# Optimization experiments

Measured on AMD Instinct MI355X. Metric: run time of the kernel, lower is better.

Reference implementation:

```python
import jax, jax.numpy as jnp
from jax import lax
import numpy as np

B, S, D, H2, V = 1024, 256, 128, 5, 50257
EPS = 1e-5


def setup_inputs() -> dict:
    key = jax.random.key(0)
    ks = jax.random.split(key, 12)
    s = 0.08  # init scale ~ 1/sqrt(D)
    return {
        "x": jax.random.randint(ks[0], (B, S), 0, V),
        "emb": jax.random.normal(ks[1], (V, D), jnp.float32) * s,
        "W_ih1": jax.random.normal(ks[2], (D, D), jnp.float32) * s,
        "b_ih1": jax.random.normal(ks[3], (D,), jnp.float32) * s,
        "W_hh1": jax.random.normal(ks[4], (D, D), jnp.float32) * s,
        "b_hh1": jax.random.normal(ks[5], (D,), jnp.float32) * s,
        "g1": jnp.ones((D,), jnp.float32),
        "be1": jnp.zeros((D,), jnp.float32),
        "W_ih2": jax.random.normal(ks[6], (H2, D), jnp.float32) * s,
        "b_ih2": jax.random.normal(ks[7], (H2,), jnp.float32) * s,
        "W_hh2": jax.random.normal(ks[8], (H2, H2), jnp.float32) * s,
        "b_hh2": jax.random.normal(ks[9], (H2,), jnp.float32) * s,
        "g2": jnp.ones((H2,), jnp.float32),
        "be2": jnp.zeros((H2,), jnp.float32),
    }


def _rnn(xproj, W_hh):
    """Vanilla tanh RNN. xproj: [B,S,H] = x @ W_ih^T + b_ih + b_hh (precomputed)."""
    h0 = jnp.zeros((xproj.shape[0], W_hh.shape[0]), xproj.dtype)

    def step(h, xt):  # xt: [B,H]
        h = jnp.tanh(xt + h @ W_hh.T)
        return h, h

    _, hs = lax.scan(step, h0, jnp.swapaxes(xproj, 0, 1))  # [S,B,H]
    return jnp.swapaxes(hs, 0, 1)  # [B,S,H]


def _ln(z, g, b):
    m = jnp.mean(z, axis=-1, keepdims=True)
    v = jnp.mean(jnp.square(z - m), axis=-1, keepdims=True)
    return (z - m) * lax.rsqrt(v + EPS) * g + b


def reference(x, emb, W_ih1, b_ih1, W_hh1, b_hh1, g1, be1,
              W_ih2, b_ih2, W_hh2, b_hh2, g2, be2):
    e = emb[x]  # [B,S,D]
    z = _rnn(e @ W_ih1.T + (b_ih1 + b_hh1), W_hh1)
    z = _ln(z, g1, be1)
    z = _rnn(z @ W_ih2.T + (b_ih2 + b_hh2), W_hh2)  # [B,S,5]
    z = _ln(z, g2, be2)
    pooled = jnp.mean(z, axis=1)  # AvgPool1d over full seq -> [B,5]
    return jax.nn.softmax(pooled, axis=1)
```

## Files before the change

### kernel.cpp

```cpp
#include <hip/hip_runtime.h>
#include <stdint.h>

#define S_LEN 256
#define DIM   128
#define EPSL  1e-5f

typedef __bf16 bf16x8 __attribute__((ext_vector_type(8)));
typedef float  f32x4  __attribute__((ext_vector_type(4)));

__device__ __forceinline__ unsigned short f2bf_bits(float f) {
  union { float f; unsigned int u; } v; v.f = f;
  unsigned int r = v.u + 0x7fffu + ((v.u >> 16) & 1u);
  return (unsigned short)(r >> 16);
}
__device__ __forceinline__ float bf2f_bits(unsigned short b) {
  union { float f; unsigned int u; } v; v.u = ((unsigned int)b) << 16; return v.f;
}
__device__ __forceinline__ unsigned f2bf_rhu(float f) {
  return (__float_as_uint(f) + 0x8000u) >> 16;
}
__device__ __forceinline__ unsigned pack_rhu(float lo, float hi) {
  return __builtin_amdgcn_perm(__float_as_uint(hi) + 0x8000u,
                               __float_as_uint(lo) + 0x8000u, 0x07060302u);
}
__device__ __forceinline__ float tanh_fast(float x) {
  float e = __expf(2.f * x);
  return 1.f - 2.f * __builtin_amdgcn_rcpf(e + 1.f);
}

template<int CTRL>
__device__ __forceinline__ float dpp_rot_add(float v) {
  int r = __builtin_amdgcn_update_dpp(0, __float_as_int(v), CTRL, 0xF, 0xF, true);
  return v + __int_as_float(r);
}
template<int CTRL>
__device__ __forceinline__ float dpp_rot_max(float v) {
  int r = __builtin_amdgcn_update_dpp(0, __float_as_int(v), CTRL, 0xF, 0xF, true);
  return fmaxf(v, __int_as_float(r));
}
__device__ __forceinline__ float dpp_sum16(float v) {
  v = dpp_rot_add<0x124>(v); v = dpp_rot_add<0x128>(v);
  v = dpp_rot_add<0x39>(v);  v = dpp_rot_add<0x4E>(v);
  return v;
}
__device__ __forceinline__ float dpp_max16(float v) {
  v = dpp_rot_max<0x124>(v); v = dpp_rot_max<0x128>(v);
  v = dpp_rot_max<0x39>(v);  v = dpp_rot_max<0x4E>(v);
  return v;
}
template<int CTRL>
__device__ __forceinline__ void red_level7(float& s, float& sq, float* d) {
  s  = dpp_rot_add<CTRL>(s);
  sq = dpp_rot_add<CTRL>(sq);
#pragma unroll
  for (int j = 0; j < 5; j++) d[j] = dpp_rot_add<CTRL>(d[j]);
}
template<int JJ>
__device__ __forceinline__ float bcast16(float v) {
  int r = __builtin_amdgcn_ds_swizzle(__float_as_int(v), (JJ << 5) | 0x10);
  return __int_as_float(r);
}

union Frag8 { unsigned short us[8]; bf16x8 v; int4 i4; };

__global__ __launch_bounds__(512, 2)
void rnn_main(const int* __restrict__ x, const float* __restrict__ emb,
              const float* __restrict__ Wih1, const float* __restrict__ bih1,
              const float* __restrict__ Whh1, const float* __restrict__ bhh1,
              const float* __restrict__ g1, const float* __restrict__ be1,
              const float* __restrict__ Wih2, const float* __restrict__ bih2,
              const float* __restrict__ Whh2, const float* __restrict__ bhh2,
              const float* __restrict__ g2, const float* __restrict__ be2,
              unsigned short* __restrict__ hout, int* flags,
              float* __restrict__ out)
{
  __shared__ __align__(16) unsigned short h_bf[2][16 * 128];
  __shared__ __align__(16) unsigned short e_bf[2][16 * 128];
  __shared__ int x_tile[16 * 256];
  __shared__ __align__(16) float p_lds[8][2][32][8];

  const int tid  = threadIdx.x;
  const int wave = tid >> 6;
  const int lane = tid & 63;
  const int l15  = lane & 15;
  const int q    = lane >> 4;

  if (blockIdx.x < 64) {
    const int r0 = blockIdx.x * 16;
    for (int i = tid; i < 16 * 256; i += 512)
      x_tile[i] = x[(size_t)(r0 + (i >> 8)) * S_LEN + (i & 255)];
    for (int i = tid; i < 16 * 128; i += 512) h_bf[1][i] = 0;

    const int n1 = wave * 16 + l15;
    const float bias1v = bih1[n1] + bhh1[n1];
    bf16x8 wh[4], wih[4];
#pragma unroll
    for (int kt = 0; kt < 4; kt++) {
      int k0 = kt * 32 + q * 8;
      Frag8 fh, fa;
#pragma unroll
      for (int j = 0; j < 8; j++) {
        fh.us[j] = f2bf_bits(Whh1[n1 * DIM + k0 + j]);
        fa.us[j] = f2bf_bits(Wih1[n1 * DIM + k0 + j]);
      }
      wh[kt] = fh.v; wih[kt] = fa.v;
    }

    const bool stage_role = (wave >= 4);
    float pf[2][8];
    const int gm   = (wave & 3) * 4 + q;
    const int goct = l15;
    const int gdst = gm * 128 + ((goct ^ gm) & 15) * 8;
    __syncthreads();

    if (stage_role) {
      float ta[8], tb[8];
      { int xid = x_tile[gm * 256 + 0];
        const float* pe = emb + (size_t)xid * DIM + goct * 8;
#pragma unroll
        for (int j = 0; j < 8; j++) ta[j] = pe[j]; }
      { int xid = x_tile[gm * 256 + 1];
        const float* pe = emb + (size_t)xid * DIM + goct * 8;
#pragma unroll
        for (int j = 0; j < 8; j++) tb[j] = pe[j]; }
      { int xid = x_tile[gm * 256 + 2];
        const float* pe = emb + (size_t)xid * DIM + goct * 8;
#pragma unroll
        for (int j = 0; j < 8; j++) pf[0][j] = pe[j]; }
      { int xid = x_tile[gm * 256 + 3];
        const float* pe = emb + (size_t)xid * DIM + goct * 8;
#pragma unroll
        for (int j = 0; j < 8; j++) pf[1][j] = pe[j]; }
      Frag8 pa, pb;
#pragma unroll
      for (int j = 0; j < 8; j++) { pa.us[j] = f2bf_bits(ta[j]); pb.us[j] = f2bf_bits(tb[j]); }
      *(int4*)&e_bf[0][gdst] = pa.i4;
      *(int4*)&e_bf[1][gdst] = pb.i4;
    }
    __syncthreads();

    f32x4 xpacc = {bias1v, bias1v, bias1v, bias1v};
#pragma unroll
    for (int kt = 0; kt < 4; kt++) {
      int sw = (((kt * 4 + q) ^ l15) & 15) * 8;
      bf16x8 ae = *(const bf16x8*)&e_bf[0][l15 * 128 + sw];
      xpacc = __builtin_amdgcn_mfma_f32_16x16x32_bf16(ae, wih[kt], xpacc, 0, 0, 0);
    }
    asm volatile("s_waitcnt lgkmcnt(0)\n\ts_barrier" ::: "memory");

#pragma unroll 2
    for (int t = 0; t < S_LEN; t++) {
      f32x4 acc = xpacc;
      {
        const int rb = (t + 1) & 1;
#pragma unroll
        for (int kt = 0; kt < 4; kt++) {
          int sw = (((kt * 4 + q) ^ l15) & 15) * 8;
          bf16x8 ahf = *(const bf16x8*)&h_bf[rb][l15 * 128 + sw];
          acc = __builtin_amdgcn_mfma_f32_16x16x32_bf16(ahf, wh[kt], acc, 0, 0, 0);
        }
        const int wb = t & 1;
        const int oct = n1 >> 3;
#pragma unroll
        for (int r = 0; r < 4; r++) {
          int row = q * 4 + r;
          unsigned short us = (unsigned short)f2bf_rhu(tanh_fast(acc[r]));
          h_bf[wb][row * 128 + ((oct ^ row) & 15) * 8 + (n1 & 7)] = us;
          hout[((size_t)(r0 + row) * S_LEN + t) * DIM + n1] = us;
        }
      }

      if (t + 1 < S_LEN) {
        f32x4 a = {bias1v, bias1v, bias1v, bias1v};
#pragma unroll
        for (int kt = 0; kt < 4; kt++) {
          int sw = (((kt * 4 + q) ^ l15) & 15) * 8;
          bf16x8 ae = *(const bf16x8*)&e_bf[(t + 1) & 1][l15 * 128 + sw];
          a = __builtin_amdgcn_mfma_f32_16x16x32_bf16(ae, wih[kt], a, 0, 0, 0);
        }
        xpacc = a;
      }

      if (stage_role) {
        if (t + 2 < S_LEN) {
          int4 pk;
          pk.x = pack_rhu(pf[t & 1][0], pf[t & 1][1]);
          pk.y = pack_rhu(pf[t & 1][2], pf[t & 1][3]);
          pk.z = pack_rhu(pf[t & 1][4], pf[t & 1][5]);
          pk.w = pack_rhu(pf[t & 1][6], pf[t & 1][7]);
          *(int4*)&e_bf[t & 1][gdst] = pk;
        }
        if (t + 4 < S_LEN) {
          int xid = x_tile[gm * 256 + t + 4];
          const float* pe = emb + (size_t)xid * DIM + goct * 8;
#pragma unroll
          for (int j = 0; j < 8; j++) pf[t & 1][j] = pe[j];
        }
      }
      if (flags != nullptr && (t & 31) == 31)
        asm volatile("s_waitcnt vmcnt(0)" ::: "memory");
      asm volatile("s_waitcnt lgkmcnt(0)\n\ts_barrier" ::: "memory");
      if (flags != nullptr && (t & 31) == 31 && tid == 0)
        __hip_atomic_store(&flags[blockIdx.x * 8 + (t >> 5)], (t >> 5) + 1,
                           __ATOMIC_RELEASE, __HIP_MEMORY_SCOPE_AGENT);
    }
  } else {
    const int bt = blockIdx.x - 64;
    float w2g[5][8], Gs[5], Bs[5], wrow[5];
#pragma unroll
    for (int j = 0; j < 8; j++) {
      int c = l15 * 8 + j;
      float gc = g1[c];
#pragma unroll
      for (int jj = 0; jj < 5; jj++) w2g[jj][j] = Wih2[jj * DIM + c] * gc;
    }
#pragma unroll
    for (int jj = 0; jj < 5; jj++) { Gs[jj] = 0.f; Bs[jj] = 0.f; }
    for (int c = 0; c < DIM; c++) {
      float gc = g1[c], bc = be1[c];
#pragma unroll
      for (int jj = 0; jj < 5; jj++) {
        float w = Wih2[jj * DIM + c];
        Gs[jj] += w * gc; Bs[jj] += w * bc;
      }
    }
    const float validf = (l15 < 5) ? 1.f : 0.f;
    float t2_l = 0.f, g2_l = 0.f, be2_l = 0.f;
    if (l15 < 5) {
      t2_l = bih2[l15] + bhh2[l15];
      g2_l = g2[l15]; be2_l = be2[l15];
#pragma unroll
      for (int jj = 0; jj < 5; jj++) wrow[jj] = Whh2[l15 * 5 + jj];
    } else {
#pragma unroll
      for (int jj = 0; jj < 5; jj++) wrow[jj] = 0.f;
    }
    float h2rep[5] = {0, 0, 0, 0, 0}, pool_l = 0.f;
    const int row_l = 2 * wave + (q & 1);
    const unsigned short* hb =
        hout + (size_t)(bt * 16 + row_l) * S_LEN * DIM;
    const int idx = (l15 < 5) ? l15 : 0;

    for (int c8 = 0; c8 < 8; c8++) {
      if (tid == 0) {
        while (__hip_atomic_load(&flags[bt * 8 + c8], __ATOMIC_RELAXED,
                                 __HIP_MEMORY_SCOPE_AGENT) < c8 + 1)
          __builtin_amdgcn_s_sleep(2);
      }
      __syncthreads();
      __builtin_amdgcn_fence(__ATOMIC_ACQUIRE, "agent");
      for (int tt = 0; tt < 16; tt++) {
        int toff = tt * 2 + (q >> 1);
        uint4 cur = *(const uint4*)(hb + (size_t)(c8 * 32 + toff) * DIM + l15 * 8);
        float hv[8];
        hv[0] = __uint_as_float(cur.x << 16); hv[1] = __uint_as_float(cur.x & 0xffff0000u);
        hv[2] = __uint_as_float(cur.y << 16); hv[3] = __uint_as_float(cur.y & 0xffff0000u);
        hv[4] = __uint_as_float(cur.z << 16); hv[5] = __uint_as_float(cur.z & 0xffff0000u);
        hv[6] = __uint_as_float(cur.w << 16); hv[7] = __uint_as_float(cur.w & 0xffff0000u);
        float s = 0.f, sq = 0.f, d[5] = {0, 0, 0, 0, 0};
#pragma unroll
        for (int j = 0; j < 8; j++) {
          float v = hv[j];
          s += v; sq += v * v;
#pragma unroll
          for (int jj = 0; jj < 5; jj++) d[jj] = fmaf(w2g[jj][j], v, d[jj]);
        }
        red_level7<0x124>(s, sq, d);
        red_level7<0x128>(s, sq, d);
        red_level7<0x39>(s, sq, d);
        red_level7<0x4E>(s, sq, d);
        float mean = s * (1.f / 128.f);
        float var  = sq * (1.f / 128.f) - mean * mean;
        float rstd = rsqrtf(var + EPSL);
        float p[5];
#pragma unroll
        for (int jj = 0; jj < 5; jj++)
          p[jj] = rstd * (d[jj] - mean * Gs[jj]) + Bs[jj];
        float psel = (l15 == 0) ? p[0] : (l15 == 1) ? p[1] :
                     (l15 == 2) ? p[2] : (l15 == 3) ? p[3] : p[4];
        if (l15 < 5) p_lds[wave][q & 1][toff][l15] = psel;
      }
      asm volatile("s_waitcnt lgkmcnt(0)" ::: "memory");
      for (int s = 0; s < 32; s++) {
        float pv = p_lds[wave][q & 1][s][idx];
        float a = pv + t2_l;
#pragma unroll
        for (int jj = 0; jj < 5; jj++) a = fmaf(wrow[jj], h2rep[jj], a);
        float xn = tanh_fast(a);
        float s2 = dpp_sum16(xn * validf) * 0.2f;
        float dd = xn - s2;
        float v2 = dpp_sum16(dd * dd * validf) * 0.2f;
        float r2 = rsqrtf(v2 + EPSL);
        pool_l += dd * r2 * g2_l + be2_l;
        h2rep[0] = bcast16<0>(xn); h2rep[1] = bcast16<1>(xn);
        h2rep[2] = bcast16<2>(xn); h2rep[3] = bcast16<3>(xn);
        h2rep[4] = bcast16<4>(xn);
      }
    }
    float lg = pool_l * (1.f / 256.f);
    float mx = dpp_max16((l15 < 5) ? lg : -3.0e38f);
    float e  = (l15 < 5) ? __expf(lg - mx) : 0.f;
    float sm = dpp_sum16(e);
    if (q < 2 && l15 < 5)
      out[(size_t)(bt * 16 + row_l) * 5 + l15] = e / sm;
  }
}

__global__ __launch_bounds__(256, 2)
void rnn_tail_r11(const unsigned short* __restrict__ hall,
                  const float* __restrict__ g1,  const float* __restrict__ be1,
                  const float* __restrict__ Wih2, const float* __restrict__ bih2,
                  const float* __restrict__ Whh2, const float* __restrict__ bhh2,
                  const float* __restrict__ g2,  const float* __restrict__ be2,
                  float* __restrict__ out)
{
  __shared__ float p_lds[4][4][8];
  const int tid  = threadIdx.x;
  const int wave = tid >> 6;
  const int lane = tid & 63;
  const int l15  = lane & 15;
  const int q    = lane >> 4;
  const int b    = blockIdx.x * 4 + wave;

  float w2g[5][8], Gs[5], Bs[5], wrow[5];
#pragma unroll
  for (int j = 0; j < 8; j++) {
    int c = l15 * 8 + j;
    float gc = g1[c];
#pragma unroll
    for (int jj = 0; jj < 5; jj++) w2g[jj][j] = Wih2[jj * DIM + c] * gc;
  }
#pragma unroll
  for (int jj = 0; jj < 5; jj++) { Gs[jj] = 0.f; Bs[jj] = 0.f; }
  for (int c = 0; c < DIM; c++) {
    float gc = g1[c], bc = be1[c];
#pragma unroll
    for (int jj = 0; jj < 5; jj++) {
      float w = Wih2[jj * DIM + c];
      Gs[jj] += w * gc; Bs[jj] += w * bc;
    }
  }
  const float validf = (l15 < 5) ? 1.f : 0.f;
  float t2_l = 0.f, g2_l = 0.f, be2_l = 0.f;
  if (l15 < 5) {
    t2_l = bih2[l15] + bhh2[l15];
    g2_l = g2[l15]; be2_l = be2[l15];
#pragma unroll
    for (int jj = 0; jj < 5; jj++) wrow[jj] = Whh2[l15 * 5 + jj];
  } else {
#pragma unroll
    for (int jj = 0; jj < 5; jj++) wrow[jj] = 0.f;
  }
  float h2rep[5];
#pragma unroll
  for (int jj = 0; jj < 5; jj++) h2rep[jj] = 0.f;
  float pool_l = 0.f;

  const unsigned short* hb = hall + (size_t)b * S_LEN * DIM;
  uint4 hpre = *(const uint4*)(hb + (size_t)q * DIM + l15 * 8);

  for (int t0 = 0; t0 < S_LEN; t0 += 4) {
    uint4 cur = hpre;
    if (t0 + 4 < S_LEN)
      hpre = *(const uint4*)(hb + (size_t)(t0 + 4 + q) * DIM + l15 * 8);
    float hv[8];
    hv[0] = __uint_as_float(cur.x << 16); hv[1] = __uint_as_float(cur.x & 0xffff0000u);
    hv[2] = __uint_as_float(cur.y << 16); hv[3] = __uint_as_float(cur.y & 0xffff0000u);
    hv[4] = __uint_as_float(cur.z << 16); hv[5] = __uint_as_float(cur.z & 0xffff0000u);
    hv[6] = __uint_as_float(cur.w << 16); hv[7] = __uint_as_float(cur.w & 0xffff0000u);
    float s = 0.f, sq = 0.f, d[5] = {0, 0, 0, 0, 0};
#pragma unroll
    for (int j = 0; j < 8; j++) {
      float v = hv[j];
      s += v; sq += v * v;
#pragma unroll
      for (int jj = 0; jj < 5; jj++) d[jj] = fmaf(w2g[jj][j], v, d[jj]);
    }
    red_level7<0x124>(s, sq, d);
    red_level7<0x128>(s, sq, d);
    red_level7<0x39>(s, sq, d);
    red_level7<0x4E>(s, sq, d);
    float mean = s * (1.f / 128.f);
    float var  = sq * (1.f / 128.f) - mean * mean;
    float rstd = rsqrtf(var + EPSL);
    float p[5];
#pragma unroll
    for (int jj = 0; jj < 5; jj++)
      p[jj] = rstd * (d[jj] - mean * Gs[jj]) + Bs[jj];
    float psel = (l15 == 0) ? p[0] : (l15 == 1) ? p[1] :
                 (l15 == 2) ? p[2] : (l15 == 3) ? p[3] : p[4];
    if (l15 < 5) p_lds[wave][q][l15] = psel;
    asm volatile("s_waitcnt lgkmcnt(0)" ::: "memory");
    const int idx = (l15 < 5) ? l15 : 0;
#pragma unroll
    for (int g = 0; g < 4; g++) {
      float pv = p_lds[wave][g][idx];
      float a = pv + t2_l;
#pragma unroll
      for (int jj = 0; jj < 5; jj++) a = fmaf(wrow[jj], h2rep[jj], a);
      float xn = tanh_fast(a);
      float s2 = dpp_sum16(xn * validf) * 0.2f;
      float dd = xn - s2;
      float v2 = dpp_sum16(dd * dd * validf) * 0.2f;
      float r2 = rsqrtf(v2 + EPSL);
      pool_l += dd * r2 * g2_l + be2_l;
      h2rep[0] = bcast16<0>(xn); h2rep[1] = bcast16<1>(xn);
      h2rep[2] = bcast16<2>(xn); h2rep[3] = bcast16<3>(xn);
      h2rep[4] = bcast16<4>(xn);
    }
  }

  float lg = pool_l * (1.f / 256.f);
  float mx = dpp_max16((l15 < 5) ? lg : -3.0e38f);
  float e  = (l15 < 5) ? __expf(lg - mx) : 0.f;
  float sm = dpp_sum16(e);
  if (q == 0 && l15 < 5) out[(size_t)b * 5 + l15] = e / sm;
}

extern "C" void kernel_launch(void* const* d_in, const int* in_sizes, int n_in,
                              void* d_out, int out_size, void* d_ws, size_t ws_size,
                              hipStream_t stream) {
  (void)in_sizes; (void)n_in; (void)out_size;
  const int*   x    = (const int*)  d_in[0];
  const float* emb  = (const float*)d_in[1];
  const float* Wih1 = (const float*)d_in[2];
  const float* bih1 = (const float*)d_in[3];
  const float* Whh1 = (const float*)d_in[4];
  const float* bhh1 = (const float*)d_in[5];
  const float* g1   = (const float*)d_in[6];
  const float* be1  = (const float*)d_in[7];
  const float* Wih2 = (const float*)d_in[8];
  const float* bih2 = (const float*)d_in[9];
  const float* Whh2 = (const float*)d_in[10];
  const float* bhh2 = (const float*)d_in[11];
  const float* g2   = (const float*)d_in[12];
  const float* be2  = (const float*)d_in[13];
  float* out = (float*)d_out;

  const size_t HBYTES = (size_t)1024 * S_LEN * DIM * 2;
  const size_t FBYTES = 64 * 8 * sizeof(int);
  unsigned short* hws = (unsigned short*)d_ws;

  if (ws_size >= HBYTES + 4096) {
    int* flags = (int*)((char*)d_ws + HBYTES);
    rnn_main<<<dim3(128), dim3(512), 0, stream>>>(
        x, emb, Wih1, bih1, Whh1, bhh1, g1, be1,
        Wih2, bih2, Whh2, bhh2, g2, be2, hws, flags, out);
    (void)FBYTES;
  } else {
    rnn_main<<<dim3(64), dim3(512), 0, stream>>>(
        x, emb, Wih1, bih1, Whh1, bhh1, g1, be1,
        Wih2, bih2, Whh2, bhh2, g2, be2, hws, nullptr, out);
    rnn_tail_r11<<<dim3(256), dim3(256), 0, stream>>>(
        hws, g1, be1, Wih2, bih2, Whh2, bhh2, g2, be2, out);
  }
}
```

Measured before the change: 257.1 us.

## Split recurrence and input projection into separate wave groups with 1024-thread blocks

Doubles the block to 16 waves. Waves 0-7 now only run the recurrent h@W_hh MFMA chain. Waves 8-15 compute the next step's input projection and stage embeddings, handing it over through a new double-buffered xp_lds buffer. The recurrent chain also splits its four MFMAs into two independent accumulators to shorten the dependency chain. In exchange, the per-step barrier now spans 16 waves and each step adds an LDS round-trip. Half the waves in the consumer blocks sit idle.

```diff
diff --git a/kernel.cpp b/kernel.cpp
--- a/kernel.cpp
+++ b/kernel.cpp
@@ -63,57 +63,67 @@
 
 union Frag8 { unsigned short us[8]; bf16x8 v; int4 i4; };
 
-__global__ __launch_bounds__(512, 2)
-void rnn_main(const int* __restrict__ x, const float* __restrict__ emb,
-              const float* __restrict__ Wih1, const float* __restrict__ bih1,
-              const float* __restrict__ Whh1, const float* __restrict__ bhh1,
-              const float* __restrict__ g1, const float* __restrict__ be1,
-              const float* __restrict__ Wih2, const float* __restrict__ bih2,
-              const float* __restrict__ Whh2, const float* __restrict__ bhh2,
-              const float* __restrict__ g2, const float* __restrict__ be2,
-              unsigned short* __restrict__ hout, int* flags,
-              float* __restrict__ out)
+__global__ __launch_bounds__(1024, 4)
+void rnn_main2(const int* __restrict__ x, const float* __restrict__ emb,
+               const float* __restrict__ Wih1, const float* __restrict__ bih1,
+               const float* __restrict__ Whh1, const float* __restrict__ bhh1,
+               const float* __restrict__ g1, const float* __restrict__ be1,
+               const float* __restrict__ Wih2, const float* __restrict__ bih2,
+               const float* __restrict__ Whh2, const float* __restrict__ bhh2,
+               const float* __restrict__ g2, const float* __restrict__ be2,
+               unsigned short* __restrict__ hout, int* flags,
+               float* __restrict__ out)
 {
   __shared__ __align__(16) unsigned short h_bf[2][16 * 128];
   __shared__ __align__(16) unsigned short e_bf[2][16 * 128];
   __shared__ int x_tile[16 * 256];
+  __shared__ __align__(16) float xp_lds[2][128][16];
   __shared__ __align__(16) float p_lds[8][2][32][8];
 
-  const int tid  = threadIdx.x;
-  const int wave = tid >> 6;
-  const int lane = tid & 63;
-  const int l15  = lane & 15;
-  const int q    = lane >> 4;
+  const int tid   = threadIdx.x;
+  const int wave  = tid >> 6;
+  const int waveu = __builtin_amdgcn_readfirstlane(wave);
+  const int lane  = tid & 63;
+  const int l15   = lane & 15;
+  const int q     = lane >> 4;
 
   if (blockIdx.x < 64) {
     const int r0 = blockIdx.x * 16;
-    for (int i = tid; i < 16 * 256; i += 512)
+    for (int i = tid; i < 16 * 256; i += 1024)
       x_tile[i] = x[(size_t)(r0 + (i >> 8)) * S_LEN + (i & 255)];
-    for (int i = tid; i < 16 * 128; i += 512) h_bf[1][i] = 0;
-
-    const int n1 = wave * 16 + l15;
-    const float bias1v = bih1[n1] + bhh1[n1];
-    bf16x8 wh[4], wih[4];
-#pragma unroll
-    for (int kt = 0; kt < 4; kt++) {
-      int k0 = kt * 32 + q * 8;
-      Frag8 fh, fa;
-#pragma unroll
-      for (int j = 0; j < 8; j++) {
-        fh.us[j] = f2bf_bits(Whh1[n1 * DIM + k0 + j]);
-        fa.us[j] = f2bf_bits(Wih1[n1 * DIM + k0 + j]);
-      }
-      wh[kt] = fh.v; wih[kt] = fa.v;
-    }
-
-    const bool stage_role = (wave >= 4);
-    float pf[2][8];
+    for (int i = tid; i < 16 * 128; i += 1024) h_bf[1][i] = 0;
+
+    const int n1 = (waveu < 8 ? wave : wave - 8) * 16 + l15;
+    bf16x8 wreg[4];
+    float bias1v = 0.f;
+    if (waveu < 8) {
+#pragma unroll
+      for (int kt = 0; kt < 4; kt++) {
+        int k0 = kt * 32 + q * 8;
+        Frag8 f;
+#pragma unroll
+        for (int j = 0; j < 8; j++) f.us[j] = f2bf_bits(Whh1[n1 * DIM + k0 + j]);
+        wreg[kt] = f.v;
+      }
+    } else {
+      bias1v = bih1[n1] + bhh1[n1];
+#pragma unroll
+      for (int kt = 0; kt < 4; kt++) {
+        int k0 = kt * 32 + q * 8;
+        Frag8 f;
+#pragma unroll
+        for (int j = 0; j < 8; j++) f.us[j] = f2bf_bits(Wih1[n1 * DIM + k0 + j]);
+        wreg[kt] = f.v;
+      }
+    }
+
     const int gm   = (wave & 3) * 4 + q;
     const int goct = l15;
     const int gdst = gm * 128 + ((goct ^ gm) & 15) * 8;
+    float pf[2][8];
     __syncthreads();
 
-    if (stage_role) {
+    if (waveu >= 8 && waveu < 12) {
       float ta[8], tb[8];
       { int xid = x_tile[gm * 256 + 0];
         const float* pe = emb + (size_t)xid * DIM + goct * 8;
@@ -139,25 +149,38 @@
     }
     __syncthreads();
 
-    f32x4 xpacc = {bias1v, bias1v, bias1v, bias1v};
-#pragma unroll
-    for (int kt = 0; kt < 4; kt++) {
-      int sw = (((kt * 4 + q) ^ l15) & 15) * 8;
-      bf16x8 ae = *(const bf16x8*)&e_bf[0][l15 * 128 + sw];
-      xpacc = __builtin_amdgcn_mfma_f32_16x16x32_bf16(ae, wih[kt], xpacc, 0, 0, 0);
-    }
-    asm volatile("s_waitcnt lgkmcnt(0)\n\ts_barrier" ::: "memory");
+    if (waveu >= 8) {
+      f32x4 a = {bias1v, bias1v, bias1v, bias1v};
+#pragma unroll
+      for (int kt = 0; kt < 4; kt++) {
+        int sw = (((kt * 4 + q) ^ l15) & 15) * 8;
+        bf16x8 ae = *(const bf16x8*)&e_bf[0][l15 * 128 + sw];
+        a = __builtin_amdgcn_mfma_f32_16x16x32_bf16(ae, wreg[kt], a, 0, 0, 0);
+      }
+      *(f32x4*)&xp_lds[0][n1][q * 4] = a;
+    }
+    __syncthreads();
 
 #pragma unroll 2
     for (int t = 0; t < S_LEN; t++) {
-      f32x4 acc = xpacc;
-      {
+      if (waveu < 8) {
         const int rb = (t + 1) & 1;
-#pragma unroll
-        for (int kt = 0; kt < 4; kt++) {
-          int sw = (((kt * 4 + q) ^ l15) & 15) * 8;
-          bf16x8 ahf = *(const bf16x8*)&h_bf[rb][l15 * 128 + sw];
-          acc = __builtin_amdgcn_mfma_f32_16x16x32_bf16(ahf, wh[kt], acc, 0, 0, 0);
+        f32x4 acc  = *(const f32x4*)&xp_lds[t & 1][n1][q * 4];
+        f32x4 accb = {0.f, 0.f, 0.f, 0.f};
+        {
+          int sw0 = ((q ^ l15) & 15) * 8;
+          int sw1 = (((4 + q) ^ l15) & 15) * 8;
+          int sw2 = (((8 + q) ^ l15) & 15) * 8;
+          int sw3 = (((12 + q) ^ l15) & 15) * 8;
+          bf16x8 a0 = *(const bf16x8*)&h_bf[rb][l15 * 128 + sw0];
+          bf16x8 a1 = *(const bf16x8*)&h_bf[rb][l15 * 128 + sw1];
+          bf16x8 a2 = *(const bf16x8*)&h_bf[rb][l15 * 128 + sw2];
+          bf16x8 a3 = *(const bf16x8*)&h_bf[rb][l15 * 128 + sw3];
+          acc  = __builtin_amdgcn_mfma_f32_16x16x32_bf16(a0, wreg[0], acc,  0, 0, 0);
+          accb = __builtin_amdgcn_mfma_f32_16x16x32_bf16(a2, wreg[2], accb, 0, 0, 0);
+          acc  = __builtin_amdgcn_mfma_f32_16x16x32_bf16(a1, wreg[1], acc,  0, 0, 0);
+          accb = __builtin_amdgcn_mfma_f32_16x16x32_bf16(a3, wreg[3], accb, 0, 0, 0);
+          acc += accb;
         }
         const int wb = t & 1;
         const int oct = n1 >> 3;
@@ -168,36 +191,35 @@
           h_bf[wb][row * 128 + ((oct ^ row) & 15) * 8 + (n1 & 7)] = us;
           hout[((size_t)(r0 + row) * S_LEN + t) * DIM + n1] = us;
         }
-      }
-
-      if (t + 1 < S_LEN) {
-        f32x4 a = {bias1v, bias1v, bias1v, bias1v};
-#pragma unroll
-        for (int kt = 0; kt < 4; kt++) {
-          int sw = (((kt * 4 + q) ^ l15) & 15) * 8;
-          bf16x8 ae = *(const bf16x8*)&e_bf[(t + 1) & 1][l15 * 128 + sw];
-          a = __builtin_amdgcn_mfma_f32_16x16x32_bf16(ae, wih[kt], a, 0, 0, 0);
-        }
-        xpacc = a;
-      }
-
-      if (stage_role) {
-        if (t + 2 < S_LEN) {
-          int4 pk;
-          pk.x = pack_rhu(pf[t & 1][0], pf[t & 1][1]);
-          pk.y = pack_rhu(pf[t & 1][2], pf[t & 1][3]);
-          pk.z = pack_rhu(pf[t & 1][4], pf[t & 1][5]);
-          pk.w = pack_rhu(pf[t & 1][6], pf[t & 1][7]);
-          *(int4*)&e_bf[t & 1][gdst] = pk;
-        }
-        if (t + 4 < S_LEN) {
-          int xid = x_tile[gm * 256 + t + 4];
-          const float* pe = emb + (size_t)xid * DIM + goct * 8;
-#pragma unroll
-          for (int j = 0; j < 8; j++) pf[t & 1][j] = pe[j];
-        }
-      }
-      if (flags != nullptr && (t & 31) == 31)
+      } else {
+        if (t + 1 < S_LEN) {
+          f32x4 a = {bias1v, bias1v, bias1v, bias1v};
+#pragma unroll
+          for (int kt = 0; kt < 4; kt++) {
+            int sw = (((kt * 4 + q) ^ l15) & 15) * 8;
+            bf16x8 ae = *(const bf16x8*)&e_bf[(t + 1) & 1][l15 * 128 + sw];
+            a = __builtin_amdgcn_mfma_f32_16x16x32_bf16(ae, wreg[kt], a, 0, 0, 0);
+          }
+          *(f32x4*)&xp_lds[(t + 1) & 1][n1][q * 4] = a;
+        }
+        if (waveu < 12) {
+          if (t + 2 < S_LEN) {
+            int4 pk;
+            pk.x = pack_rhu(pf[t & 1][0], pf[t & 1][1]);
+            pk.y = pack_rhu(pf[t & 1][2], pf[t & 1][3]);
+            pk.z = pack_rhu(pf[t & 1][4], pf[t & 1][5]);
+            pk.w = pack_rhu(pf[t & 1][6], pf[t & 1][7]);
+            *(int4*)&e_bf[t & 1][gdst] = pk;
+          }
+          if (t + 4 < S_LEN) {
+            int xid = x_tile[gm * 256 + t + 4];
+            const float* pe = emb + (size_t)xid * DIM + goct * 8;
+#pragma unroll
+            for (int j = 0; j < 8; j++) pf[t & 1][j] = pe[j];
+          }
+        }
+      }
+      if (flags != nullptr && (t & 31) == 31 && waveu < 8)
         asm volatile("s_waitcnt vmcnt(0)" ::: "memory");
       asm volatile("s_waitcnt lgkmcnt(0)\n\ts_barrier" ::: "memory");
       if (flags != nullptr && (t & 31) == 31 && tid == 0)
@@ -236,7 +258,7 @@
       for (int jj = 0; jj < 5; jj++) wrow[jj] = 0.f;
     }
     float h2rep[5] = {0, 0, 0, 0, 0}, pool_l = 0.f;
-    const int row_l = 2 * wave + (q & 1);
+    const int row_l = 2 * (wave & 7) + (q & 1);
     const unsigned short* hb =
         hout + (size_t)(bt * 16 + row_l) * S_LEN * DIM;
     const int idx = (l15 < 5) ? l15 : 0;
@@ -249,60 +271,64 @@
       }
       __syncthreads();
       __builtin_amdgcn_fence(__ATOMIC_ACQUIRE, "agent");
-      for (int tt = 0; tt < 16; tt++) {
-        int toff = tt * 2 + (q >> 1);
-        uint4 cur = *(const uint4*)(hb + (size_t)(c8 * 32 + toff) * DIM + l15 * 8);
-        float hv[8];
-        hv[0] = __uint_as_float(cur.x << 16); hv[1] = __uint_as_float(cur.x & 0xffff0000u);
-        hv[2] = __uint_as_float(cur.y << 16); hv[3] = __uint_as_float(cur.y & 0xffff0000u);
-        hv[4] = __uint_as_float(cur.z << 16); hv[5] = __uint_as_float(cur.z & 0xffff0000u);
-        hv[6] = __uint_as_float(cur.w << 16); hv[7] = __uint_as_float(cur.w & 0xffff0000u);
-        float s = 0.f, sq = 0.f, d[5] = {0, 0, 0, 0, 0};
-#pragma unroll
-        for (int j = 0; j < 8; j++) {
-          float v = hv[j];
-          s += v; sq += v * v;
-#pragma unroll
-          for (int jj = 0; jj < 5; jj++) d[jj] = fmaf(w2g[jj][j], v, d[jj]);
-        }
-        red_level7<0x124>(s, sq, d);
-        red_level7<0x128>(s, sq, d);
-        red_level7<0x39>(s, sq, d);
-        red_level7<0x4E>(s, sq, d);
-        float mean = s * (1.f / 128.f);
-        float var  = sq * (1.f / 128.f) - mean * mean;
-        float rstd = rsqrtf(var + EPSL);
-        float p[5];
-#pragma unroll
-        for (int jj = 0; jj < 5; jj++)
-          p[jj] = rstd * (d[jj] - mean * Gs[jj]) + Bs[jj];
-        float psel = (l15 == 0) ? p[0] : (l15 == 1) ? p[1] :
-                     (l15 == 2) ? p[2] : (l15 == 3) ? p[3] : p[4];
-        if (l15 < 5) p_lds[wave][q & 1][toff][l15] = psel;
-      }
-      asm volatile("s_waitcnt lgkmcnt(0)" ::: "memory");
-      for (int s = 0; s < 32; s++) {
-        float pv = p_lds[wave][q & 1][s][idx];
-        float a = pv + t2_l;
-#pragma unroll
-        for (int jj = 0; jj < 5; jj++) a = fmaf(wrow[jj], h2rep[jj], a);
-        float xn = tanh_fast(a);
-        float s2 = dpp_sum16(xn * validf) * 0.2f;
-        float dd = xn - s2;
-        float v2 = dpp_sum16(dd * dd * validf) * 0.2f;
-        float r2 = rsqrtf(v2 + EPSL);
-        pool_l += dd * r2 * g2_l + be2_l;
-        h2rep[0] = bcast16<0>(xn); h2rep[1] = bcast16<1>(xn);
-        h2rep[2] = bcast16<2>(xn); h2rep[3] = bcast16<3>(xn);
-        h2rep[4] = bcast16<4>(xn);
-      }
-    }
-    float lg = pool_l * (1.f / 256.f);
-    float mx = dpp_max16((l15 < 5) ? lg : -3.0e38f);
-    float e  = (l15 < 5) ? __expf(lg - mx) : 0.f;
-    float sm = dpp_sum16(e);
-    if (q < 2 && l15 < 5)
-      out[(size_t)(bt * 16 + row_l) * 5 + l15] = e / sm;
+      if (waveu < 8) {
+        for (int tt = 0; tt < 16; tt++) {
+          int toff = tt * 2 + (q >> 1);
+          uint4 cur = *(const uint4*)(hb + (size_t)(c8 * 32 + toff) * DIM + l15 * 8);
+          float hv[8];
+          hv[0] = __uint_as_float(cur.x << 16); hv[1] = __uint_as_float(cur.x & 0xffff0000u);
+          hv[2] = __uint_as_float(cur.y << 16); hv[3] = __uint_as_float(cur.y & 0xffff0000u);
+          hv[4] = __uint_as_float(cur.z << 16); hv[5] = __uint_as_float(cur.z & 0xffff0000u);
+          hv[6] = __uint_as_float(cur.w << 16); hv[7] = __uint_as_float(cur.w & 0xffff0000u);
+          float s = 0.f, sq = 0.f, d[5] = {0, 0, 0, 0, 0};
+#pragma unroll
+          for (int j = 0; j < 8; j++) {
+            float v = hv[j];
+            s += v; sq += v * v;
+#pragma unroll
+            for (int jj = 0; jj < 5; jj++) d[jj] = fmaf(w2g[jj][j], v, d[jj]);
+          }
+          red_level7<0x124>(s, sq, d);
+          red_level7<0x128>(s, sq, d);
+          red_level7<0x39>(s, sq, d);
+          red_level7<0x4E>(s, sq, d);
+          float mean = s * (1.f / 128.f);
+          float var  = sq * (1.f / 128.f) - mean * mean;
+          float rstd = rsqrtf(var + EPSL);
+          float p[5];
+#pragma unroll
+          for (int jj = 0; jj < 5; jj++)
+            p[jj] = rstd * (d[jj] - mean * Gs[jj]) + Bs[jj];
+          float psel = (l15 == 0) ? p[0] : (l15 == 1) ? p[1] :
+                       (l15 == 2) ? p[2] : (l15 == 3) ? p[3] : p[4];
+          if (l15 < 5) p_lds[wave & 7][q & 1][toff][l15] = psel;
+        }
+        asm volatile("s_waitcnt lgkmcnt(0)" ::: "memory");
+        for (int s = 0; s < 32; s++) {
+          float pv = p_lds[wave & 7][q & 1][s][idx];
+          float a = pv + t2_l;
+#pragma unroll
+          for (int jj = 0; jj < 5; jj++) a = fmaf(wrow[jj], h2rep[jj], a);
+          float xn = tanh_fast(a);
+          float s2 = dpp_sum16(xn * validf) * 0.2f;
+          float dd = xn - s2;
+          float v2 = dpp_sum16(dd * dd * validf) * 0.2f;
+          float r2 = rsqrtf(v2 + EPSL);
+          pool_l += dd * r2 * g2_l + be2_l;
+          h2rep[0] = bcast16<0>(xn); h2rep[1] = bcast16<1>(xn);
+          h2rep[2] = bcast16<2>(xn); h2rep[3] = bcast16<3>(xn);
+          h2rep[4] = bcast16<4>(xn);
+        }
+      }
+    }
+    if (waveu < 8) {
+      float lg = pool_l * (1.f / 256.f);
+      float mx = dpp_max16((l15 < 5) ? lg : -3.0e38f);
+      float e  = (l15 < 5) ? __expf(lg - mx) : 0.f;
+      float sm = dpp_sum16(e);
+      if (q < 2 && l15 < 5)
+        out[(size_t)(bt * 16 + row_l) * 5 + l15] = e / sm;
+    }
   }
 }
 
@@ -438,17 +464,15 @@
   float* out = (float*)d_out;
 
   const size_t HBYTES = (size_t)1024 * S_LEN * DIM * 2;
-  const size_t FBYTES = 64 * 8 * sizeof(int);
   unsigned short* hws = (unsigned short*)d_ws;
 
   if (ws_size >= HBYTES + 4096) {
     int* flags = (int*)((char*)d_ws + HBYTES);
-    rnn_main<<<dim3(128), dim3(512), 0, stream>>>(
+    rnn_main2<<<dim3(128), dim3(1024), 0, stream>>>(
         x, emb, Wih1, bih1, Whh1, bhh1, g1, be1,
         Wih2, bih2, Whh2, bhh2, g2, be2, hws, flags, out);
-    (void)FBYTES;
   } else {
-    rnn_main<<<dim3(64), dim3(512), 0, stream>>>(
+    rnn_main2<<<dim3(64), dim3(1024), 0, stream>>>(
         x, emb, Wih1, bih1, Whh1, bhh1, g1, be1,
         Wih2, bih2, Whh2, bhh2, g2, be2, hws, nullptr, out);
     rnn_tail_r11<<<dim3(256), dim3(256), 0, stream>>>(
```

Result: slower. 318.4 us (+23.8%).

## Restructure layer-1 RNN into two-wave blocks with LDS ring of precomputed input projections

Applied to the files above, without the earlier changes.

The layer-1 recurrence now runs in 128-thread blocks of two waves. Each wave owns 64 hidden columns and keeps all W_ih fragments in registers. Input projections are computed several steps ahead into a six-entry LDS ring, so the serial step only reads xproj plus four h-tile loads. The step also splits its MFMA chain into two accumulators to shorten dependency latency, and hidden-state writeback to global uses coalesced 16-byte rows instead of scattered shorts. The consumer blocks are remapped to 128 blocks of 8 rows each, which raises register pressure and changes the flag-publishing cadence.

```diff
diff --git a/kernel.cpp b/kernel.cpp
--- a/kernel.cpp
+++ b/kernel.cpp
@@ -4,6 +4,7 @@
 #define S_LEN 256
 #define DIM   128
 #define EPSL  1e-5f
+#define NCORE 64
 
 typedef __bf16 bf16x8 __attribute__((ext_vector_type(8)));
 typedef float  f32x4  __attribute__((ext_vector_type(4)));
@@ -13,9 +14,6 @@
   unsigned int r = v.u + 0x7fffu + ((v.u >> 16) & 1u);
   return (unsigned short)(r >> 16);
 }
-__device__ __forceinline__ float bf2f_bits(unsigned short b) {
-  union { float f; unsigned int u; } v; v.u = ((unsigned int)b) << 16; return v.f;
-}
 __device__ __forceinline__ unsigned f2bf_rhu(float f) {
   return (__float_as_uint(f) + 0x8000u) >> 16;
 }
@@ -63,149 +61,175 @@
 
 union Frag8 { unsigned short us[8]; bf16x8 v; int4 i4; };
 
-__global__ __launch_bounds__(512, 2)
-void rnn_main(const int* __restrict__ x, const float* __restrict__ emb,
-              const float* __restrict__ Wih1, const float* __restrict__ bih1,
-              const float* __restrict__ Whh1, const float* __restrict__ bhh1,
-              const float* __restrict__ g1, const float* __restrict__ be1,
-              const float* __restrict__ Wih2, const float* __restrict__ bih2,
-              const float* __restrict__ Whh2, const float* __restrict__ bhh2,
-              const float* __restrict__ g2, const float* __restrict__ be2,
-              unsigned short* __restrict__ hout, int* flags,
-              float* __restrict__ out)
+__global__ __launch_bounds__(128, 1)
+void rnn_fused(const int* __restrict__ x, const float* __restrict__ emb,
+               const float* __restrict__ Wih1, const float* __restrict__ bih1,
+               const float* __restrict__ Whh1, const float* __restrict__ bhh1,
+               const float* __restrict__ g1, const float* __restrict__ be1,
+               const float* __restrict__ Wih2, const float* __restrict__ bih2,
+               const float* __restrict__ Whh2, const float* __restrict__ bhh2,
+               const float* __restrict__ g2, const float* __restrict__ be2,
+               unsigned short* __restrict__ hout, int* flags,
+               float* __restrict__ out)
 {
+  __shared__ __align__(16) float xp_ring[6][8][64][4];
   __shared__ __align__(16) unsigned short h_bf[2][16 * 128];
-  __shared__ __align__(16) unsigned short e_bf[2][16 * 128];
-  __shared__ int x_tile[16 * 256];
-  __shared__ __align__(16) float p_lds[8][2][32][8];
+  __shared__ __align__(16) float p_lds[2][4][32][8];
 
   const int tid  = threadIdx.x;
-  const int wave = tid >> 6;
+  const int uw   = tid >> 6;
   const int lane = tid & 63;
   const int l15  = lane & 15;
   const int q    = lane >> 4;
 
-  if (blockIdx.x < 64) {
-    const int r0 = blockIdx.x * 16;
-    for (int i = tid; i < 16 * 256; i += 512)
-      x_tile[i] = x[(size_t)(r0 + (i >> 8)) * S_LEN + (i & 255)];
-    for (int i = tid; i < 16 * 128; i += 512) h_bf[1][i] = 0;
-
-    const int n1 = wave * 16 + l15;
-    const float bias1v = bih1[n1] + bhh1[n1];
-    bf16x8 wh[4], wih[4];
-#pragma unroll
-    for (int kt = 0; kt < 4; kt++) {
-      int k0 = kt * 32 + q * 8;
-      Frag8 fh, fa;
-#pragma unroll
-      for (int j = 0; j < 8; j++) {
-        fh.us[j] = f2bf_bits(Whh1[n1 * DIM + k0 + j]);
-        fa.us[j] = f2bf_bits(Wih1[n1 * DIM + k0 + j]);
-      }
-      wh[kt] = fh.v; wih[kt] = fa.v;
-    }
-
-    const bool stage_role = (wave >= 4);
-    float pf[2][8];
-    const int gm   = (wave & 3) * 4 + q;
-    const int goct = l15;
-    const int gdst = gm * 128 + ((goct ^ gm) & 15) * 8;
-    __syncthreads();
-
-    if (stage_role) {
-      float ta[8], tb[8];
-      { int xid = x_tile[gm * 256 + 0];
-        const float* pe = emb + (size_t)xid * DIM + goct * 8;
-#pragma unroll
-        for (int j = 0; j < 8; j++) ta[j] = pe[j]; }
-      { int xid = x_tile[gm * 256 + 1];
-        const float* pe = emb + (size_t)xid * DIM + goct * 8;
-#pragma unroll
-        for (int j = 0; j < 8; j++) tb[j] = pe[j]; }
-      { int xid = x_tile[gm * 256 + 2];
-        const float* pe = emb + (size_t)xid * DIM + goct * 8;
-#pragma unroll
-        for (int j = 0; j < 8; j++) pf[0][j] = pe[j]; }
-      { int xid = x_tile[gm * 256 + 3];
-        const float* pe = emb + (size_t)xid * DIM + goct * 8;
-#pragma unroll
-        for (int j = 0; j < 8; j++) pf[1][j] = pe[j]; }
-      Frag8 pa, pb;
-#pragma unroll
-      for (int j = 0; j < 8; j++) { pa.us[j] = f2bf_bits(ta[j]); pb.us[j] = f2bf_bits(tb[j]); }
-      *(int4*)&e_bf[0][gdst] = pa.i4;
-      *(int4*)&e_bf[1][gdst] = pb.i4;
-    }
-    __syncthreads();
-
-    f32x4 xpacc = {bias1v, bias1v, bias1v, bias1v};
-#pragma unroll
-    for (int kt = 0; kt < 4; kt++) {
-      int sw = (((kt * 4 + q) ^ l15) & 15) * 8;
-      bf16x8 ae = *(const bf16x8*)&e_bf[0][l15 * 128 + sw];
-      xpacc = __builtin_amdgcn_mfma_f32_16x16x32_bf16(ae, wih[kt], xpacc, 0, 0, 0);
-    }
-    asm volatile("s_waitcnt lgkmcnt(0)\n\ts_barrier" ::: "memory");
-
-#pragma unroll 2
-    for (int t = 0; t < S_LEN; t++) {
-      f32x4 acc = xpacc;
-      {
-        const int rb = (t + 1) & 1;
-#pragma unroll
-        for (int kt = 0; kt < 4; kt++) {
-          int sw = (((kt * 4 + q) ^ l15) & 15) * 8;
-          bf16x8 ahf = *(const bf16x8*)&h_bf[rb][l15 * 128 + sw];
-          acc = __builtin_amdgcn_mfma_f32_16x16x32_bf16(ahf, wh[kt], acc, 0, 0, 0);
-        }
-        const int wb = t & 1;
-        const int oct = n1 >> 3;
+  if (blockIdx.x < NCORE) {
+    const int r0u = blockIdx.x * 16;
+    for (int i = tid; i < 16 * 128; i += 128) h_bf[1][i] = 0;
+
+    bf16x8 whh[4][4]; bf16x8 wih[8][4]; float biasx[8];
+#pragma unroll
+    for (int n = 0; n < 4; n++) {
+      int d = uw * 64 + n * 16 + l15;
+#pragma unroll
+      for (int kt = 0; kt < 4; kt++) {
+        Frag8 f;
+#pragma unroll
+        for (int j = 0; j < 8; j++)
+          f.us[j] = f2bf_bits(Whh1[d * DIM + kt * 32 + q * 8 + j]);
+        whh[n][kt] = f.v;
+      }
+    }
+#pragma unroll
+    for (int n8 = 0; n8 < 8; n8++) {
+      int d = n8 * 16 + l15;
+      biasx[n8] = bih1[d] + bhh1[d];
+#pragma unroll
+      for (int kt = 0; kt < 4; kt++) {
+        Frag8 f;
+#pragma unroll
+        for (int j = 0; j < 8; j++)
+          f.us[j] = f2bf_bits(Wih1[d * DIM + kt * 32 + q * 8 + j]);
+        wih[n8][kt] = f.v;
+      }
+    }
+
+    float4 eld[8];
+    int xid_pref = 0;
+
+    auto gather = [&](int tq) {
+      int xid = x[(size_t)(r0u + l15) * S_LEN + tq];
+      const float* pe = emb + (size_t)xid * DIM + q * 8;
+#pragma unroll
+      for (int kt = 0; kt < 4; kt++) {
+        eld[kt * 2]     = *(const float4*)(pe + kt * 32);
+        eld[kt * 2 + 1] = *(const float4*)(pe + kt * 32 + 4);
+      }
+    };
+    auto produce = [&](int entry) {
+      Frag8 af[4];
+#pragma unroll
+      for (int kt = 0; kt < 4; kt++) {
+        af[kt].i4.x = (int)pack_rhu(eld[kt * 2].x,     eld[kt * 2].y);
+        af[kt].i4.y = (int)pack_rhu(eld[kt * 2].z,     eld[kt * 2].w);
+        af[kt].i4.z = (int)pack_rhu(eld[kt * 2 + 1].x, eld[kt * 2 + 1].y);
+        af[kt].i4.w = (int)pack_rhu(eld[kt * 2 + 1].z, eld[kt * 2 + 1].w);
+      }
+#pragma unroll
+      for (int n8 = 0; n8 < 8; n8++) {
+        f32x4 a = {biasx[n8], biasx[n8], biasx[n8], biasx[n8]};
+#pragma unroll
+        for (int kt = 0; kt < 4; kt++)
+          a = __builtin_amdgcn_mfma_f32_16x16x32_bf16(af[kt].v, wih[n8][kt], a, 0, 0, 0);
+        *(f32x4*)&xp_ring[entry][n8][lane][0] = a;
+      }
+    };
+    auto serial_step = [&](int T, int RM) {
+      const int rb = (T + 1) & 1, wb = T & 1;
+      f32x4 xpv[4];
+#pragma unroll
+      for (int n = 0; n < 4; n++)
+        xpv[n] = *(const f32x4*)&xp_ring[RM][uw * 4 + n][lane][0];
+      bf16x8 a0 = *(const bf16x8*)&h_bf[rb][l15 * 128 + ((( 0 + q) ^ l15) & 15) * 8];
+      bf16x8 a1 = *(const bf16x8*)&h_bf[rb][l15 * 128 + ((( 4 + q) ^ l15) & 15) * 8];
+      bf16x8 a2 = *(const bf16x8*)&h_bf[rb][l15 * 128 + ((( 8 + q) ^ l15) & 15) * 8];
+      bf16x8 a3 = *(const bf16x8*)&h_bf[rb][l15 * 128 + (((12 + q) ^ l15) & 15) * 8];
+#pragma unroll
+      for (int n = 0; n < 4; n++) {
+        f32x4 acc = xpv[n]; f32x4 accb = {0.f, 0.f, 0.f, 0.f};
+        acc  = __builtin_amdgcn_mfma_f32_16x16x32_bf16(a0, whh[n][0], acc,  0, 0, 0);
+        accb = __builtin_amdgcn_mfma_f32_16x16x32_bf16(a2, whh[n][2], accb, 0, 0, 0);
+        acc  = __builtin_amdgcn_mfma_f32_16x16x32_bf16(a1, whh[n][1], acc,  0, 0, 0);
+        accb = __builtin_amdgcn_mfma_f32_16x16x32_bf16(a3, whh[n][3], accb, 0, 0, 0);
+        acc += accb;
+        const int c = uw * 64 + n * 16 + l15, oct = c >> 3;
 #pragma unroll
         for (int r = 0; r < 4; r++) {
           int row = q * 4 + r;
-          unsigned short us = (unsigned short)f2bf_rhu(tanh_fast(acc[r]));
-          h_bf[wb][row * 128 + ((oct ^ row) & 15) * 8 + (n1 & 7)] = us;
-          hout[((size_t)(r0 + row) * S_LEN + t) * DIM + n1] = us;
+          h_bf[wb][row * 128 + ((oct ^ row) & 15) * 8 + (c & 7)] =
+              (unsigned short)f2bf_rhu(tanh_fast(acc[r]));
         }
       }
-
-      if (t + 1 < S_LEN) {
-        f32x4 a = {bias1v, bias1v, bias1v, bias1v};
-#pragma unroll
-        for (int kt = 0; kt < 4; kt++) {
-          int sw = (((kt * 4 + q) ^ l15) & 15) * 8;
-          bf16x8 ae = *(const bf16x8*)&e_bf[(t + 1) & 1][l15 * 128 + sw];
-          a = __builtin_amdgcn_mfma_f32_16x16x32_bf16(ae, wih[kt], a, 0, 0, 0);
+    };
+    auto readback = [&](int T) {
+      const int hb_ = T & 1;
+#pragma unroll
+      for (int i = 0; i < 2; i++) {
+        int row = i * 8 + (lane >> 3), ol = uw * 8 + (lane & 7);
+        int4 v = *(const int4*)&h_bf[hb_][row * 128 + ((ol ^ row) & 15) * 8];
+        *(int4*)(hout + ((size_t)(r0u + row) * S_LEN + T) * DIM + ol * 8) = v;
+      }
+    };
+
+    gather(uw);      produce(uw);
+    gather(2 + uw);  produce(2 + uw);
+    gather(4 + uw);
+    xid_pref = x[(size_t)(r0u + l15) * S_LEN + 6 + uw];
+    int em = 4 + uw;
+    asm volatile("s_waitcnt lgkmcnt(0)\n\ts_barrier" ::: "memory");
+
+    int rm = 0;
+    for (int tp = 0; tp < S_LEN / 2; tp++) {
+      const int t0 = 2 * tp, t1 = t0 + 1;
+      if (t0 > 0) readback(t0 - 1);
+      serial_step(t0, rm);
+      rm = (rm == 5) ? 0 : rm + 1;
+      {
+        int ts = t0 + 4 + uw;
+        if (ts < S_LEN) { produce(em); em += 2; if (em >= 6) em -= 6; }
+        int tn = t0 + 6 + uw;
+        if (tn < S_LEN) {
+          const float* pe = emb + (size_t)xid_pref * DIM + q * 8;
+#pragma unroll
+          for (int kt = 0; kt < 4; kt++) {
+            eld[kt * 2]     = *(const float4*)(pe + kt * 32);
+            eld[kt * 2 + 1] = *(const float4*)(pe + kt * 32 + 4);
+          }
+          if (tn + 2 < S_LEN)
+            xid_pref = x[(size_t)(r0u + l15) * S_LEN + tn + 2];
         }
-        xpacc = a;
-      }
-
-      if (stage_role) {
-        if (t + 2 < S_LEN) {
-          int4 pk;
-          pk.x = pack_rhu(pf[t & 1][0], pf[t & 1][1]);
-          pk.y = pack_rhu(pf[t & 1][2], pf[t & 1][3]);
-          pk.z = pack_rhu(pf[t & 1][4], pf[t & 1][5]);
-          pk.w = pack_rhu(pf[t & 1][6], pf[t & 1][7]);
-          *(int4*)&e_bf[t & 1][gdst] = pk;
-        }
-        if (t + 4 < S_LEN) {
-          int xid = x_tile[gm * 256 + t + 4];
-          const float* pe = emb + (size_t)xid * DIM + goct * 8;
-#pragma unroll
-          for (int j = 0; j < 8; j++) pf[t & 1][j] = pe[j];
-        }
-      }
-      if (flags != nullptr && (t & 31) == 31)
+      }
+      if (flags != nullptr && t0 > 0 && (t0 & 31) == 0)
         asm volatile("s_waitcnt vmcnt(0)" ::: "memory");
       asm volatile("s_waitcnt lgkmcnt(0)\n\ts_barrier" ::: "memory");
-      if (flags != nullptr && (t & 31) == 31 && tid == 0)
-        __hip_atomic_store(&flags[blockIdx.x * 8 + (t >> 5)], (t >> 5) + 1,
+      if (flags != nullptr && t0 > 0 && (t0 & 31) == 0 && tid == 0)
+        __hip_atomic_store(&flags[blockIdx.x * 8 + (t0 >> 5) - 1], t0 >> 5,
                            __ATOMIC_RELEASE, __HIP_MEMORY_SCOPE_AGENT);
+      readback(t0);
+      serial_step(t1, rm);
+      rm = (rm == 5) ? 0 : rm + 1;
+      asm volatile("s_waitcnt lgkmcnt(0)\n\ts_barrier" ::: "memory");
+    }
+    readback(S_LEN - 1);
+    if (flags != nullptr) {
+      asm volatile("s_waitcnt vmcnt(0)" ::: "memory");
+      __syncthreads();
+      if (tid == 0)
+        __hip_atomic_store(&flags[blockIdx.x * 8 + 7], 8,
+                           __ATOMIC_RELEASE, __HIP_MEMORY_SCOPE_AGENT);
     }
   } else {
-    const int bt = blockIdx.x - 64;
+    const int bt = blockIdx.x - NCORE;
+    const int u  = bt >> 1;
     float w2g[5][8], Gs[5], Bs[5], wrow[5];
 #pragma unroll
     for (int j = 0; j < 8; j++) {
@@ -225,7 +249,8 @@
       }
     }
     const float validf = (l15 < 5) ? 1.f : 0.f;
-    float t2_l = 0.f, g2_l = 0.f, be2_l = 0.f;
+    float t2_l = 0.f, g2_l = 0.f, be2_l = 0.f, wrow_z[5];
+    (void)wrow_z;
     if (l15 < 5) {
       t2_l = bih2[l15] + bhh2[l15];
       g2_l = g2[l15]; be2_l = be2[l15];
@@ -236,22 +261,20 @@
       for (int jj = 0; jj < 5; jj++) wrow[jj] = 0.f;
     }
     float h2rep[5] = {0, 0, 0, 0, 0}, pool_l = 0.f;
-    const int row_l = 2 * wave + (q & 1);
-    const unsigned short* hb =
-        hout + (size_t)(bt * 16 + row_l) * S_LEN * DIM;
+    const int rowg = bt * 8 + uw * 4 + q;
+    const unsigned short* hb = hout + (size_t)rowg * S_LEN * DIM;
     const int idx = (l15 < 5) ? l15 : 0;
 
     for (int c8 = 0; c8 < 8; c8++) {
       if (tid == 0) {
-        while (__hip_atomic_load(&flags[bt * 8 + c8], __ATOMIC_RELAXED,
+        while (__hip_atomic_load(&flags[u * 8 + c8], __ATOMIC_RELAXED,
                                  __HIP_MEMORY_SCOPE_AGENT) < c8 + 1)
           __builtin_amdgcn_s_sleep(2);
       }
       __syncthreads();
       __builtin_amdgcn_fence(__ATOMIC_ACQUIRE, "agent");
-      for (int tt = 0; tt < 16; tt++) {
-        int toff = tt * 2 + (q >> 1);
-        uint4 cur = *(const uint4*)(hb + (size_t)(c8 * 32 + toff) * DIM + l15 * 8);
+      for (int tt = 0; tt < 32; tt++) {
+        uint4 cur = *(const uint4*)(hb + (size_t)(c8 * 32 + tt) * DIM + l15 * 8);
         float hv[8];
         hv[0] = __uint_as_float(cur.x << 16); hv[1] = __uint_as_float(cur.x & 0xffff0000u);
         hv[2] = __uint_as_float(cur.y << 16); hv[3] = __uint_as_float(cur.y & 0xffff0000u);
@@ -278,11 +301,11 @@
           p[jj] = rstd * (d[jj] - mean * Gs[jj]) + Bs[jj];
         float psel = (l15 == 0) ? p[0] : (l15 == 1) ? p[1] :
                      (l15 == 2) ? p[2] : (l15 == 3) ? p[3] : p[4];
-        if (l15 < 5) p_lds[wave][q & 1][toff][l15] = psel;
+        if (l15 < 5) p_lds[uw][q][tt][l15] = psel;
       }
       asm volatile("s_waitcnt lgkmcnt(0)" ::: "memory");
       for (int s = 0; s < 32; s++) {
-        float pv = p_lds[wave][q & 1][s][idx];
+        float pv = p_lds[uw][q][s][idx];
         float a = pv + t2_l;
 #pragma unroll
         for (int jj = 0; jj < 5; jj++) a = fmaf(wrow[jj], h2rep[jj], a);
@@ -301,8 +324,7 @@
     float mx = dpp_max16((l15 < 5) ? lg : -3.0e38f);
     float e  = (l15 < 5) ? __expf(lg - mx) : 0.f;
     float sm = dpp_sum16(e);
-    if (q < 2 && l15 < 5)
-      out[(size_t)(bt * 16 + row_l) * 5 + l15] = e / sm;
+    if (l15 < 5) out[(size_t)rowg * 5 + l15] = e / sm;
   }
 }
 
@@ -438,17 +460,15 @@
   float* out = (float*)d_out;
 
   const size_t HBYTES = (size_t)1024 * S_LEN * DIM * 2;
-  const size_t FBYTES = 64 * 8 * sizeof(int);
   unsigned short* hws = (unsigned short*)d_ws;
 
   if (ws_size >= HBYTES + 4096) {
     int* flags = (int*)((char*)d_ws + HBYTES);
-    rnn_main<<<dim3(128), dim3(512), 0, stream>>>(
+    rnn_fused<<<dim3(NCORE + 128), dim3(128), 0, stream>>>(
         x, emb, Wih1, bih1, Whh1, bhh1, g1, be1,
         Wih2, bih2, Whh2, bhh2, g2, be2, hws, flags, out);
-    (void)FBYTES;
   } else {
-    rnn_main<<<dim3(64), dim3(512), 0, stream>>>(
+    rnn_fused<<<dim3(NCORE), dim3(128), 0, stream>>>(
         x, emb, Wih1, bih1, Whh1, bhh1, g1, be1,
         Wih2, bih2, Whh2, bhh2, g2, be2, hws, nullptr, out);
     rnn_tail_r11<<<dim3(256), dim3(256), 0, stream>>>(
```

After: 394.5 us. 1.53x slower.
